# Kernel tuning notes

Hardware: AMD Instinct MI355X
Metric: run time of the kernel (lower is better)

The kernel has to match this reference:

```python
import jax, jax.numpy as jnp
import numpy as np

DN = ('NCHW', 'OIHW', 'NCHW')
BN_EPS = 1e-5


def _conv3x3(x, w, b):
    y = jax.lax.conv_general_dilated(x, w, (1, 1), ((1, 1), (1, 1)), dimension_numbers=DN)
    return y + b[None, :, None, None]


def _bn(x, g, b, m, v):
    # eval-mode BatchNorm with running stats
    scale = g * jax.lax.rsqrt(v + BN_EPS)
    return (x - m[None, :, None, None]) * scale[None, :, None, None] + b[None, :, None, None]


def _bilinear_gather(x, py, px):
    # x: [B,C,H,W]; py, px: [B,K,H,W] float sampling coords (zero padding outside)
    B, C, H, W = x.shape
    y0 = jnp.floor(py)
    x0 = jnp.floor(px)
    wy = py - y0
    wx = px - x0
    y0i = y0.astype(jnp.int32)
    x0i = x0.astype(jnp.int32)
    xf = x.reshape(B, C, H * W)

    def corner(yi, xi, wgt):
        valid = (yi >= 0) & (yi < H) & (xi >= 0) & (xi < W)
        idx = jnp.clip(yi, 0, H - 1) * W + jnp.clip(xi, 0, W - 1)  # [B,K,H,W]
        g = jax.vmap(lambda xb, ib: xb[:, ib])(xf, idx)            # [B,C,K,H,W]
        return g * (wgt * valid.astype(x.dtype))[:, None]

    v = corner(y0i, x0i, (1 - wy) * (1 - wx))
    v = v + corner(y0i, x0i + 1, (1 - wy) * wx)
    v = v + corner(y0i + 1, x0i, wy * (1 - wx))
    v = v + corner(y0i + 1, x0i + 1, wy * wx)
    return v  # [B,C,K,H,W]


def _deform_conv(x, offset, mask, w):
    # modulated deformable conv: 3x3, stride 1, pad 1, dilation 1, groups=1, dg=1
    B, C, H, W = x.shape
    K = 9
    ky = jnp.arange(K) // 3 - 1  # kernel row offsets
    kx = jnp.arange(K) % 3 - 1   # kernel col offsets
    dy = offset[:, :K]           # [B,K,H,W]
    dx = offset[:, K:]
    py = dy + (ky[:, None, None] + jnp.arange(H)[None, :, None]).astype(x.dtype)
    px = dx + (kx[:, None, None] + jnp.arange(W)[None, None, :]).astype(x.dtype)
    val = _bilinear_gather(x, py, px) * mask[:, None]  # [B,C,K,H,W]
    O = w.shape[0]
    return jnp.einsum('bckhw,ock->bohw', val, w.reshape(O, C, K))


def _deconv(x, w):
    # ConvTranspose2d k=4 s=2 p=1, bias=False; torch weight layout [Cin, Cout, 4, 4]
    wk = jnp.flip(w, (2, 3)).transpose(1, 0, 2, 3)  # [Cout, Cin, 4, 4]
    return jax.lax.conv_general_dilated(x, wk, (1, 1), ((2, 2), (2, 2)),
                                        lhs_dilation=(2, 2), dimension_numbers=DN)


def setup_inputs() -> dict:
    key = jax.random.key(0)
    ks = jax.random.split(key, 14)
    B, Cin, Cout, H, W = 8, 256, 256, 64, 64
    x = jax.random.normal(ks[0], (B, Cin, H, W), jnp.float32)
    w_off = jax.random.normal(ks[1], (27, Cin, 3, 3), jnp.float32) * 0.01
    b_off = jnp.zeros((27,), jnp.float32)
    w_dcn = jax.random.normal(ks[2], (Cout, Cin, 3, 3), jnp.float32) * (2.0 / (Cin * 9)) ** 0.5
    gamma1 = 1.0 + 0.1 * jax.random.normal(ks[3], (Cout,), jnp.float32)
    beta1 = 0.1 * jax.random.normal(ks[4], (Cout,), jnp.float32)
    mean1 = 0.1 * jax.random.normal(ks[5], (Cout,), jnp.float32)
    var1 = jax.random.uniform(ks[6], (Cout,), jnp.float32, 0.5, 1.5)
    w_up = jax.random.normal(ks[7], (Cout, Cout, 4, 4), jnp.float32) * 0.05
    gamma2 = 1.0 + 0.1 * jax.random.normal(ks[8], (Cout,), jnp.float32)
    beta2 = 0.1 * jax.random.normal(ks[9], (Cout,), jnp.float32)
    mean2 = 0.1 * jax.random.normal(ks[10], (Cout,), jnp.float32)
    var2 = jax.random.uniform(ks[11], (Cout,), jnp.float32, 0.5, 1.5)
    return dict(x=x, w_off=w_off, b_off=b_off, w_dcn=w_dcn,
                gamma1=gamma1, beta1=beta1, mean1=mean1, var1=var1,
                w_up=w_up, gamma2=gamma2, beta2=beta2, mean2=mean2, var2=var2)


def reference(x, w_off, b_off, w_dcn, gamma1, beta1, mean1, var1,
              w_up, gamma2, beta2, mean2, var2):
    offset_mask = _conv3x3(x, w_off, b_off)          # [B,27,H,W]
    ox, oy, m = jnp.split(offset_mask, 3, axis=1)
    offset = jnp.concatenate([ox, oy], axis=1)       # [B,18,H,W]
    mask = jax.nn.sigmoid(m)                         # [B,9,H,W]
    y = _deform_conv(x, offset, mask, w_dcn)
    y = jax.nn.relu(_bn(y, gamma1, beta1, mean1, var1))
    up = _deconv(y, w_up)
    up = jax.nn.relu(_bn(up, gamma2, beta2, mean2, var2))
    return (y, up)
```

## Files before the change

kernel.cpp:

```cpp
#include <hip/hip_runtime.h>
#include <cstddef>


#define B_EPS 1e-5f

typedef __bf16 bf16x8 __attribute__((ext_vector_type(8)));
typedef float f32x4 __attribute__((ext_vector_type(4)));
typedef unsigned short u16;
typedef unsigned int u32;

__device__ __forceinline__ u32 bfr(float f) {
    u32 u = __float_as_uint(f);
    return (u + 0x7FFFu + ((u >> 16) & 1u)) >> 16;
}

__device__ __forceinline__ void gather8(const float* cb2, uint4 q, int g8, f32x4* ga) {
    const float* p00 = cb2 + ((size_t)(q.x & 0xFFFFu) << 5) + g8;
    const float* p01 = cb2 + ((size_t)(q.x >> 16) << 5) + g8;
    const float* p10 = cb2 + ((size_t)(q.y & 0xFFFFu) << 5) + g8;
    const float* p11 = cb2 + ((size_t)(q.y >> 16) << 5) + g8;
    ga[0] = *(const f32x4*)p00; ga[1] = *(const f32x4*)(p00 + 4);
    ga[2] = *(const f32x4*)p01; ga[3] = *(const f32x4*)(p01 + 4);
    ga[4] = *(const f32x4*)p10; ga[5] = *(const f32x4*)(p10 + 4);
    ga[6] = *(const f32x4*)p11; ga[7] = *(const f32x4*)(p11 + 4);
}

__device__ __forceinline__ uint4 packv(uint4 q, const f32x4* ga) {
    const float w00 = __uint_as_float(q.z << 16);
    const float w01 = __uint_as_float(q.z & 0xFFFF0000u);
    const float w10 = __uint_as_float(q.w << 16);
    const float w11 = __uint_as_float(q.w & 0xFFFF0000u);
    union { bf16x8 h; uint4 u; } r;
#pragma unroll
    for (int jj = 0; jj < 4; ++jj) {
        r.h[jj]     = (__bf16)fmaf(w00, ga[0][jj], fmaf(w01, ga[2][jj], fmaf(w10, ga[4][jj], w11 * ga[6][jj])));
        r.h[4 + jj] = (__bf16)fmaf(w00, ga[1][jj], fmaf(w01, ga[3][jj], fmaf(w10, ga[5][jj], w11 * ga[7][jj])));
    }
    return r.u;
}

__global__ __launch_bounds__(256) void k_prep_wdb(const float* __restrict__ w,
                                                  u16* __restrict__ o) {
    int i = blockIdx.x * 256 + threadIdx.x;
    int kk = i & 31; int e = i >> 5;
    int oc = e & 255; int ch = e >> 8;
    int cc = ch & 7; int k = ch >> 3;
    o[i] = (u16)bfr(w[oc * 2304 + (cc * 32 + kk) * 9 + k]);
}

__global__ __launch_bounds__(256) void k_prep_wtb(const float* __restrict__ w,
                                                  u16* __restrict__ o) {
    int i = blockIdx.x * 256 + threadIdx.x;
    int kk = i & 31; int e = i >> 5;
    int oc = e & 255; e >>= 8;
    int cc = e & 31; int cls = e >> 5;
    int tap = kk >> 3, ci = cc * 8 + (kk & 7);
    int ca = cls >> 1, cb = cls & 1;
    int wr = (tap >> 1) ? (ca ? 0 : 1) : (ca ? 2 : 3);
    int wc = (tap & 1) ? (cb ? 0 : 1) : (cb ? 2 : 3);
    o[i] = (u16)bfr(w[ci * 4096 + oc * 16 + wr * 4 + wc]);
}

__global__ __launch_bounds__(256) void k_prep_wob(const float* __restrict__ w,
                                                  u16* __restrict__ o) {
    int i = blockIdx.x * 256 + threadIdx.x;
    int kk = i & 31; int e = i >> 5;
    int oc = e & 31; e >>= 5;
    int part = e & 1; int ch = e >> 1;
    int cc = ch & 7, k = ch >> 3;
    float v = (oc < 27) ? w[oc * 2304 + (cc * 32 + kk) * 9 + k] : 0.f;
    u16 hh = bfr(v);
    if (part) {
        float vh = __uint_as_float((u32)hh << 16);
        hh = (u16)bfr(v - vh);
    }
    o[i] = hh;
}

__global__ __launch_bounds__(256) void k_bn_prep(
    const float* g1, const float* be1, const float* mu1, const float* va1,
    const float* g2, const float* be2, const float* mu2, const float* va2,
    float* bnp) {
    int t = threadIdx.x;
    float s1 = g1[t] * rsqrtf(va1[t] + B_EPS);
    bnp[t] = s1; bnp[256 + t] = be1[t] - mu1[t] * s1;
    float s2 = g2[t] * rsqrtf(va2[t] + B_EPS);
    bnp[512 + t] = s2; bnp[768 + t] = be2[t] - mu2[t] * s2;
}

__global__ __launch_bounds__(256) void k_tr_x(const float* __restrict__ x,
                                              float* __restrict__ xt) {
    const int t = threadIdx.x;
    const int pg = blockIdx.x & 15;
    const int cc = (blockIdx.x >> 4) & 7;
    const int b = blockIdx.x >> 7;
    const int pix = (pg << 8) + t;
    const float* xp = x + ((size_t)b << 20) + ((size_t)(cc << 5) << 12) + pix;
    float v[32];
#pragma unroll
    for (int cl = 0; cl < 32; ++cl) v[cl] = xp[(size_t)cl << 12];
    float* op = xt + ((size_t)b << 20) + ((size_t)cc << 17) + ((size_t)pix << 5);
#pragma unroll
    for (int i = 0; i < 8; ++i)
        *(f32x4*)(op + i * 4) = *(const f32x4*)&v[i * 4];
}

__global__ __launch_bounds__(256) void k_prep_xth(const float* __restrict__ x,
                                                  u16* __restrict__ xo) {
    const int t = threadIdx.x;
    const int blk = blockIdx.x % 18;
    const int ccg = (blockIdx.x / 18) & 7;
    const int b = blockIdx.x / 144;
    const int hp = blk * 256 + t;
    if (hp >= 4356) return;
    const int h = hp / 66, w = hp % 66;
    const size_t PL = 4356u * 8u;
    u16* dh = xo + ((size_t)b * 64 + ccg * 4) * PL + (size_t)hp * 8;
    u16* dl = dh + 32 * PL;
    if (h == 0 || h == 65 || w == 0 || w == 65) {
        uint4 z = make_uint4(0, 0, 0, 0);
#pragma unroll
        for (int j = 0; j < 4; ++j) {
            *(uint4*)(dh + (size_t)j * PL) = z;
            *(uint4*)(dl + (size_t)j * PL) = z;
        }
        return;
    }
    const float* xp = x + ((size_t)b << 20) + ((size_t)(ccg * 32) << 12)
                    + ((h - 1) << 6) + (w - 1);
    u16 vh[32], vl[32];
#pragma unroll
    for (int cl = 0; cl < 32; ++cl) {
        float v = xp[(size_t)cl << 12];
        u16 hh = (u16)bfr(v);
        vh[cl] = hh;
        vl[cl] = (u16)bfr(v - __uint_as_float((u32)hh << 16));
    }
#pragma unroll
    for (int j = 0; j < 4; ++j) {
        *(uint4*)(dh + (size_t)j * PL) = *(const uint4*)&vh[j * 8];
        *(uint4*)(dl + (size_t)j * PL) = *(const uint4*)&vl[j * 8];
    }
}

__global__ __launch_bounds__(256) void k_tr_y(const float* __restrict__ y,
                                              u16* __restrict__ yt) {
    const int t = threadIdx.x;
    const int blk = blockIdx.x % 18;
    const int oc = (blockIdx.x / 18) & 7;
    const int b = blockIdx.x / 144;
    const int hp = blk * 256 + t;
    if (hp >= 4356) return;
    const int h = hp / 66, w = hp % 66;
    u16* dstb = yt + (((size_t)b * 32 + oc * 4) * 4356 + hp) * 8;
    if (h == 0 || h == 65 || w == 0 || w == 65) {
        uint4 z = make_uint4(0, 0, 0, 0);
#pragma unroll
        for (int j = 0; j < 4; ++j)
            *(uint4*)(dstb + (size_t)j * (4356 * 8)) = z;
        return;
    }
    const float* yp = y + ((size_t)b << 20) + ((size_t)(oc * 32) << 12)
                    + ((h - 1) << 6) + (w - 1);
    u16 vv[32];
#pragma unroll
    for (int cl = 0; cl < 32; ++cl) vv[cl] = (u16)bfr(yp[(size_t)cl << 12]);
#pragma unroll
    for (int j = 0; j < 4; ++j)
        *(uint4*)(dstb + (size_t)j * (4356 * 8)) = *(const uint4*)&vv[j * 8];
}

__global__ __launch_bounds__(256, 2) void k_offset_mfma(
    const u16* __restrict__ xth, const u16* __restrict__ Wob,
    const float* __restrict__ b_off, float* __restrict__ om)
{
    __shared__ float sR[4][2048];
    const int t = threadIdx.x;
    const int h0 = blockIdx.x & 63;
    const int b = blockIdx.x >> 6;
    const int wv = t >> 6;
    const int lane = t & 63;
    const int quad = lane >> 4;
    const int ln = lane & 15;
    const size_t PL = 4356u * 8u;
    const u16* xbb = xth + (size_t)b * 64 * PL;

    f32x4 acc[2][4];
#pragma unroll
    for (int i = 0; i < 2; ++i)
#pragma unroll
        for (int j = 0; j < 4; ++j) acc[i][j] = (f32x4)0.f;

#pragma unroll 3
    for (int ci = 0; ci < 18; ++ci) {
        const int ch = wv * 18 + ci;
        const int k = ch >> 3, cc = ch & 7;
        const int dy = k / 3, dx = k - dy * 3;
        const int hp = (h0 + dy) * 66 + dx + ln;
        const u16* Bh = xbb + (size_t)((cc << 2) + quad) * PL + (size_t)hp * 8;
        const u16* Bl = Bh + 32 * PL;
        const u16* Ap = Wob + ch * 2048 + ln * 32 + (quad << 3);
        bf16x8 ah[2], al[2], bh[4], bl[4];
        ah[0] = *(const bf16x8*)(Ap);
        ah[1] = *(const bf16x8*)(Ap + 512);
        al[0] = *(const bf16x8*)(Ap + 1024);
        al[1] = *(const bf16x8*)(Ap + 1536);
#pragma unroll
        for (int ni = 0; ni < 4; ++ni) {
            bh[ni] = *(const bf16x8*)(Bh + ni * 128);
            bl[ni] = *(const bf16x8*)(Bl + ni * 128);
        }
#pragma unroll
        for (int mi = 0; mi < 2; ++mi)
#pragma unroll
            for (int ni = 0; ni < 4; ++ni) {
                acc[mi][ni] = __builtin_amdgcn_mfma_f32_16x16x32_bf16(
                    ah[mi], bh[ni], acc[mi][ni], 0, 0, 0);
                acc[mi][ni] = __builtin_amdgcn_mfma_f32_16x16x32_bf16(
                    al[mi], bh[ni], acc[mi][ni], 0, 0, 0);
                acc[mi][ni] = __builtin_amdgcn_mfma_f32_16x16x32_bf16(
                    ah[mi], bl[ni], acc[mi][ni], 0, 0, 0);
            }
    }

    float* sw = &sR[wv][0];
#pragma unroll
    for (int mi = 0; mi < 2; ++mi)
#pragma unroll
        for (int ni = 0; ni < 4; ++ni)
            *(f32x4*)&sw[((mi << 2) + ni) * 256 + (lane << 2)] = acc[mi][ni];
    __syncthreads();

#pragma unroll
    for (int j = 0; j < 8; ++j) {
        int flat = (t << 3) + j;
        int e = flat >> 8;
        int rem = flat & 255;
        int l2 = rem >> 2, r = rem & 3;
        int co = ((e >> 2) << 4) + ((l2 >> 4) << 2) + r;
        if (co < 27) {
            float s = sR[0][flat] + sR[1][flat] + sR[2][flat] + sR[3][flat];
            int w = ((e & 3) << 4) + (l2 & 15);
            om[(size_t)b * 110592 + ((size_t)co << 12) + (h0 << 6) + w]
                = s + b_off[co];
        }
    }
}

__global__ __launch_bounds__(256) void k_prep_coeff(
    const float* __restrict__ om, uint4* __restrict__ cpk)
{
    int i = blockIdx.x * 256 + threadIdx.x;
    int pix = i & 4095;
    int bk = i >> 12;
    int k = bk % 9;
    int b = bk / 9;
    int h = pix >> 6, w = pix & 63;
    const float* omb = om + (size_t)b * 110592;
    float dy = omb[(k << 12) + pix];
    float dx = omb[((9 + k) << 12) + pix];
    float mr = omb[((18 + k) << 12) + pix];
    float m  = 1.f / (1.f + __expf(-mr));
    float py = dy + (float)(k / 3 - 1 + h);
    float px = dx + (float)(k % 3 - 1 + w);
    float y0f = floorf(py), x0f = floorf(px);
    float wy = py - y0f, wx = px - x0f;
    int y0 = (int)y0f, x0 = (int)x0f;
    int y1 = y0 + 1, x1 = x0 + 1;
    float vy0 = ((unsigned)y0 < 64u) ? 1.f : 0.f;
    float vy1 = ((unsigned)y1 < 64u) ? 1.f : 0.f;
    float vx0 = ((unsigned)x0 < 64u) ? 1.f : 0.f;
    float vx1 = ((unsigned)x1 < 64u) ? 1.f : 0.f;
    int cy0 = min(max(y0, 0), 63), cy1 = min(max(y1, 0), 63);
    int cx0 = min(max(x0, 0), 63), cx1 = min(max(x1, 0), 63);
    u32 xw = (u32)((cy0 << 6) + cx0) | ((u32)((cy0 << 6) + cx1) << 16);
    u32 yw = (u32)((cy1 << 6) + cx0) | ((u32)((cy1 << 6) + cx1) << 16);
    float w00 = m * (1.f - wy) * (1.f - wx) * vy0 * vx0;
    float w01 = m * (1.f - wy) * wx         * vy0 * vx1;
    float w10 = m * wy         * (1.f - wx) * vy1 * vx0;
    float w11 = m * wy         * wx         * vy1 * vx1;
    u32 zw = bfr(w00) | (bfr(w01) << 16);
    u32 ww2 = bfr(w10) | (bfr(w11) << 16);
    cpk[i] = make_uint4(xw, yw, zw, ww2);
}

__global__ __launch_bounds__(256, 2) void k_deform_mfma(
    const float* __restrict__ xt, const u16* __restrict__ Wdb,
    const uint4* __restrict__ cpk, const float* __restrict__ bnp,
    float* __restrict__ yout)
{
    __shared__ __align__(16) u16 sB[2][64 * 40];
    const int t = threadIdx.x;
    const int row = blockIdx.x & 63;
    const int b = blockIdx.x >> 6;
    const int pix0 = row << 6;
    const int p = t >> 2;
    const int g = t & 3;
    const int g8 = g << 3;
    const float* xtb = xt + ((size_t)b << 20);

    const int lane = t & 63;
    const int wv = t >> 6;
    const int quad = lane >> 4;
    const int ln = lane & 15;
    const u16* Wrow = Wdb + (size_t)(wv * 64 + ln) * 32 + quad * 8;

    f32x4 acc[4][4];
#pragma unroll
    for (int i = 0; i < 4; ++i)
#pragma unroll
        for (int j = 0; j < 4; ++j) acc[i][j] = (f32x4)0.f;

    bf16x8 afb[2][4];
    uint4 qcur = cpk[(size_t)(b * 9) * 4096 + pix0 + p];
    {
#pragma unroll
        for (int mi = 0; mi < 4; ++mi)
            afb[0][mi] = *(const bf16x8*)(Wrow + mi * 512);
        f32x4 ga[8];
        gather8(xtb, qcur, g8, ga);
        *(uint4*)&sB[0][p * 40 + g8] = packv(qcur, ga);
        __syncthreads();
    }

    for (int k = 0; k < 9; ++k) {
        uint4 qnext = qcur;
        if (k < 8) qnext = cpk[(size_t)(b * 9 + k + 1) * 4096 + pix0 + p];
#pragma unroll
        for (int cc = 0; cc < 8; ++cc) {
            const int ch = k * 8 + cc;
            const int par = cc & 1;
            const bool pre = ch < 71;
            const uint4 q = (cc == 7) ? qnext : qcur;
            f32x4 ga[8];
            if (pre) {
                const u16* Wn = Wrow + (size_t)(ch + 1) * 8192;
#pragma unroll
                for (int mi = 0; mi < 4; ++mi)
                    afb[par ^ 1][mi] = *(const bf16x8*)(Wn + mi * 512);
                gather8(xtb + ((size_t)((cc + 1) & 7) << 17), q, g8, ga);
            }
            bf16x8 bg[4];
#pragma unroll
            for (int i = 0; i < 4; ++i)
                bg[i] = *(const bf16x8*)&sB[par][(i * 16 + ln) * 40 + quad * 8];
#pragma unroll
            for (int mi = 0; mi < 4; ++mi)
#pragma unroll
                for (int ni = 0; ni < 4; ++ni)
                    acc[mi][ni] = __builtin_amdgcn_mfma_f32_16x16x32_bf16(
                        afb[par][mi], bg[ni], acc[mi][ni], 0, 0, 0);
            if (pre)
                *(uint4*)&sB[par ^ 1][p * 40 + g8] = packv(q, ga);
            __syncthreads();
        }
        qcur = qnext;
    }

    const float* sc1 = bnp;
    const float* bi1 = bnp + 256;
    float* yb2 = yout + ((size_t)b << 20);
#pragma unroll
    for (int mi = 0; mi < 4; ++mi) {
#pragma unroll
        for (int r = 0; r < 4; ++r) {
            int o = wv * 64 + mi * 16 + quad * 4 + r;
            float sc = sc1[o], bi = bi1[o];
#pragma unroll
            for (int ni = 0; ni < 4; ++ni) {
                float v = fmaxf(fmaf(acc[mi][ni][r], sc, bi), 0.f);
                yb2[((size_t)o << 12) + pix0 + ni * 16 + ln] = v;
            }
        }
    }
}

__global__ __launch_bounds__(256, 4) void k_deconv_mfma(
    const u16* __restrict__ yt, const u16* __restrict__ Wtb,
    const float* __restrict__ bnp, float* __restrict__ up)
{
    const int t = threadIdx.x;
    const int h0 = blockIdx.x & 63;
    const int cls = (blockIdx.x >> 6) & 3;
    const int b = blockIdx.x >> 8;
    const int ca = cls >> 1, cb = cls & 1;
    const int DH0 = ca ? 0 : -1, DH1 = ca ? 1 : 0;
    const int DW0 = cb ? 0 : -1, DW1 = cb ? 1 : 0;

    const int lane = t & 63;
    const int wv = t >> 6;
    const int quad = lane >> 4;
    const int ln = lane & 15;

    const int DHq = (quad >> 1) ? DH1 : DH0;
    const int DWq = (quad & 1) ? DW1 : DW0;

    const u16* ytb = yt + (size_t)b * (32u * 4356 * 8);
    const u16* Bb[4];
#pragma unroll
    for (int i = 0; i < 4; ++i) {
        int pix = i * 16 + ln;
        Bb[i] = ytb + (size_t)((h0 + DHq + 1) * 66 + (pix + DWq + 1)) * 8;
    }
    const u16* Ab = Wtb + (size_t)(cls * 32) * 8192
                  + (size_t)(wv * 64 + ln) * 32 + quad * 8;

    f32x4 acc[4][4];
#pragma unroll
    for (int i = 0; i < 4; ++i)
#pragma unroll
        for (int j = 0; j < 4; ++j) acc[i][j] = (f32x4)0.f;

#pragma unroll 2
    for (int cc = 0; cc < 32; ++cc) {
        bf16x8 af[4], bg[4];
#pragma unroll
        for (int mi = 0; mi < 4; ++mi)
            af[mi] = *(const bf16x8*)(Ab + (size_t)cc * 8192 + mi * 512);
#pragma unroll
        for (int i = 0; i < 4; ++i)
            bg[i] = *(const bf16x8*)(Bb[i] + (size_t)cc * (4356 * 8));
#pragma unroll
        for (int mi = 0; mi < 4; ++mi)
#pragma unroll
            for (int ni = 0; ni < 4; ++ni)
                acc[mi][ni] = __builtin_amdgcn_mfma_f32_16x16x32_bf16(
                    af[mi], bg[ni], acc[mi][ni], 0, 0, 0);
    }

    const float* sc2 = bnp + 512;
    const float* bi2 = bnp + 768;
    float* ub = up + ((size_t)b << 22);
    const int pr = (h0 << 1) + ca;
#pragma unroll
    for (int mi = 0; mi < 4; ++mi) {
#pragma unroll
        for (int r = 0; r < 4; ++r) {
            int o = wv * 64 + mi * 16 + quad * 4 + r;
            float sc = sc2[o], bi = bi2[o];
#pragma unroll
            for (int ni = 0; ni < 4; ++ni) {
                int qc = ((ni * 16 + ln) << 1) + cb;
                float v = fmaxf(fmaf(acc[mi][ni][r], sc, bi), 0.f);
                ub[((size_t)o << 14) + (pr << 7) + qc] = v;
            }
        }
    }
}

extern "C" void kernel_launch(void* const* d_in, const int* in_sizes, int n_in,
                              void* d_out, int out_size, void* d_ws, size_t ws_size,
                              hipStream_t stream)
{
    const float* x     = (const float*)d_in[0];
    const float* w_off = (const float*)d_in[1];
    const float* b_off = (const float*)d_in[2];
    const float* w_dcn = (const float*)d_in[3];
    const float* g1    = (const float*)d_in[4];
    const float* be1   = (const float*)d_in[5];
    const float* mu1   = (const float*)d_in[6];
    const float* va1   = (const float*)d_in[7];
    const float* w_up  = (const float*)d_in[8];
    const float* g2    = (const float*)d_in[9];
    const float* be2   = (const float*)d_in[10];
    const float* mu2   = (const float*)d_in[11];
    const float* va2   = (const float*)d_in[12];

    float* yout = (float*)d_out;
    float* up   = (float*)d_out + 8388608;
    float* xt   = up;
    u16*   xth  = (u16*)((char*)up + 33554432);

    char* ws = (char*)d_ws;
    float* om    = (float*)(ws + 0);
    uint4* cpk   = (uint4*)(ws + 3787776);
    u16*   Wob   = (u16*)  (ws + 3787776);
    u16*   Wdb   = (u16*)  (ws + 8506368);
    u16*   yt    = (u16*)  (ws + 0);
    u16*   Wtb   = (u16*)  (ws + 17842176);
    float* bnp   = (float*)(ws + 19939328);

    k_prep_wdb  <<<2304, 256, 0, stream>>>(w_dcn, Wdb);
    k_prep_wtb  <<<4096, 256, 0, stream>>>(w_up, Wtb);
    k_prep_wob  <<<576,  256, 0, stream>>>(w_off, Wob);
    k_bn_prep   <<<1,    256, 0, stream>>>(g1, be1, mu1, va1, g2, be2, mu2, va2, bnp);
    k_tr_x      <<<1024, 256, 0, stream>>>(x, xt);
    k_prep_xth  <<<1152, 256, 0, stream>>>(x, xth);
    k_offset_mfma<<<512, 256, 0, stream>>>(xth, Wob, b_off, om);
    k_prep_coeff<<<1152, 256, 0, stream>>>(om, cpk);
    k_deform_mfma<<<512, 256, 0, stream>>>(xt, Wdb, cpk, bnp, yout);
    k_tr_y      <<<1152, 256, 0, stream>>>(yout, yt);
    k_deconv_mfma<<<2048,256, 0, stream>>>(yt, Wtb, bnp, up);
}
```

Baseline: 492.6 us.

## Swizzle block-to-tile mapping and double-buffer deconv operand loads

Remaps blockIdx in the offset, deform and deconv kernels so consecutive blocks are spread across batch/class with a stride-8 interleave, likely aimed at spreading memory traffic across XCDs/L2 slices. The deconv kernel now prefetches the next channel chunk's A and B fragments into a second register buffer while the MFMAs run on the current one, to hide global load latency. To make room for the extra registers, its launch bounds drop from 4 to 3 waves per SIMD, which reduces occupancy.

```diff
diff --git a/kernel.cpp b/kernel.cpp
--- a/kernel.cpp
+++ b/kernel.cpp
@@ -176,8 +176,10 @@
 {
     __shared__ float sR[4][2048];
     const int t = threadIdx.x;
-    const int h0 = blockIdx.x & 63;
-    const int b = blockIdx.x >> 6;
+    const int bid = blockIdx.x;
+    const int lid = ((bid & 7) << 6) + (bid >> 3);
+    const int h0 = lid & 63;
+    const int b = lid >> 6;
     const int wv = t >> 6;
     const int lane = t & 63;
     const int quad = lane >> 4;
@@ -291,8 +293,10 @@
 {
     __shared__ __align__(16) u16 sB[2][64 * 40];
     const int t = threadIdx.x;
-    const int row = blockIdx.x & 63;
-    const int b = blockIdx.x >> 6;
+    const int bid = blockIdx.x;
+    const int lid = ((bid & 7) << 6) + (bid >> 3);
+    const int row = lid & 63;
+    const int b = lid >> 6;
     const int pix0 = row << 6;
     const int p = t >> 2;
     const int g = t & 3;
@@ -375,14 +379,16 @@
     }
 }
 
-__global__ __launch_bounds__(256, 4) void k_deconv_mfma(
+__global__ __launch_bounds__(256, 3) void k_deconv_mfma(
     const u16* __restrict__ yt, const u16* __restrict__ Wtb,
     const float* __restrict__ bnp, float* __restrict__ up)
 {
     const int t = threadIdx.x;
-    const int h0 = blockIdx.x & 63;
-    const int cls = (blockIdx.x >> 6) & 3;
-    const int b = blockIdx.x >> 8;
+    const int bid = blockIdx.x;
+    const int lid = ((bid & 7) << 8) + (bid >> 3);
+    const int h0 = lid & 63;
+    const int cls = (lid >> 6) & 3;
+    const int b = lid >> 8;
     const int ca = cls >> 1, cb = cls & 1;
     const int DH0 = ca ? 0 : -1, DH1 = ca ? 1 : 0;
     const int DW0 = cb ? 0 : -1, DW1 = cb ? 1 : 0;
@@ -411,21 +417,31 @@
 #pragma unroll
         for (int j = 0; j < 4; ++j) acc[i][j] = (f32x4)0.f;
 
+    bf16x8 af[2][4], bg[2][4];
+#pragma unroll
+    for (int mi = 0; mi < 4; ++mi)
+        af[0][mi] = *(const bf16x8*)(Ab + mi * 512);
+#pragma unroll
+    for (int i = 0; i < 4; ++i)
+        bg[0][i] = *(const bf16x8*)(Bb[i]);
+
 #pragma unroll 2
     for (int cc = 0; cc < 32; ++cc) {
-        bf16x8 af[4], bg[4];
-#pragma unroll
-        for (int mi = 0; mi < 4; ++mi)
-            af[mi] = *(const bf16x8*)(Ab + (size_t)cc * 8192 + mi * 512);
-#pragma unroll
-        for (int i = 0; i < 4; ++i)
-            bg[i] = *(const bf16x8*)(Bb[i] + (size_t)cc * (4356 * 8));
+        const int par = cc & 1;
+        if (cc < 31) {
+#pragma unroll
+            for (int mi = 0; mi < 4; ++mi)
+                af[par ^ 1][mi] = *(const bf16x8*)(Ab + (size_t)(cc + 1) * 8192 + mi * 512);
+#pragma unroll
+            for (int i = 0; i < 4; ++i)
+                bg[par ^ 1][i] = *(const bf16x8*)(Bb[i] + (size_t)(cc + 1) * (4356 * 8));
+        }
 #pragma unroll
         for (int mi = 0; mi < 4; ++mi)
 #pragma unroll
             for (int ni = 0; ni < 4; ++ni)
                 acc[mi][ni] = __builtin_amdgcn_mfma_f32_16x16x32_bf16(
-                    af[mi], bg[ni], acc[mi][ni], 0, 0, 0);
+                    af[par][mi], bg[par][ni], acc[mi][ni], 0, 0, 0);
     }
 
     const float* sc2 = bnp + 512;
```

After: 488.8 us. About the same (-0.8%).
